# Kernel optimization log

Measured on AMD Instinct MI355X. Metric: run time of the kernel, lower is better.

Reference implementation:

```python
import jax, jax.numpy as jnp
import numpy as np

B = 4096
D1 = 2048   # APPEARANCE_DIM
D2 = 1024   # POSE_DIM
DF = 8192   # FUSED_DIM
LN_EPS = 1e-5
L2_EPS = 1e-12


def setup_inputs() -> dict:
    key = jax.random.key(0)
    ks = jax.random.split(key, 6)
    x = jax.random.normal(ks[0], (B, D1), dtype=jnp.float32)
    y = jax.random.normal(ks[1], (B, D2), dtype=jnp.float32)
    h1 = jax.random.randint(ks[2], (D1,), 0, DF, dtype=jnp.int32)
    h2 = jax.random.randint(ks[3], (D2,), 0, DF, dtype=jnp.int32)
    s1 = (2 * jax.random.randint(ks[4], (D1,), 0, 2) - 1).astype(jnp.float32)
    s2 = (2 * jax.random.randint(ks[5], (D2,), 0, 2) - 1).astype(jnp.float32)
    gamma = jnp.ones((DF,), dtype=jnp.float32)
    beta = jnp.zeros((DF,), dtype=jnp.float32)
    return {"x": x, "y": y, "s1": s1, "s2": s2, "gamma": gamma,
            "beta": beta, "h1": h1, "h2": h2}


def count_sketch(v, h, s, out_dim):
    # v: [B, Din], h: [Din] int indices into out_dim, s: [Din] +-1 signs
    # single vectorized scatter-add along the feature axis
    return jnp.zeros((v.shape[0], out_dim), v.dtype).at[:, h].add(v * s)


def reference(x, y, s1, s2, gamma, beta, h1, h2):
    x_sk = count_sketch(x, h1, s1, DF)          # [B, DF]
    y_sk = count_sketch(y, h2, s2, DF)          # [B, DF]
    # circular convolution via FFT
    fused = jnp.fft.ifft(jnp.fft.fft(x_sk, axis=1) * jnp.fft.fft(y_sk, axis=1),
                         axis=1).real           # [B, DF]
    # LayerNorm over last dim
    mu = jnp.mean(fused, axis=-1, keepdims=True)
    var = jnp.mean(jnp.square(fused - mu), axis=-1, keepdims=True)
    normed = (fused - mu) * jax.lax.rsqrt(var + LN_EPS) * gamma + beta
    # F.normalize(p=2, dim=1)
    nrm = jnp.linalg.norm(normed, axis=1, keepdims=True)
    return normed / jnp.maximum(nrm, L2_EPS)
```

## Files before the change

kernel.cpp:

```cpp
#include <hip/hip_runtime.h>
#include <math.h>

#define BATCH 4096
#define D1 2048
#define D2 1024
#define DF 8192
#define NT 512

#define PADI(i) ((i) + ((i) >> 5))

__device__ __forceinline__ float2 cmul(float2 a, float2 b) {
    return make_float2(a.x * b.x - a.y * b.y, a.x * b.y + a.y * b.x);
}
__device__ __forceinline__ float2 cadd(float2 a, float2 b) { return make_float2(a.x + b.x, a.y + b.y); }
__device__ __forceinline__ float2 csub(float2 a, float2 b) { return make_float2(a.x - b.x, a.y - b.y); }

#define RT_C 0.92387953251128674f
#define RT_S 0.38268343236508977f
#define RT_H 0.70710678118654752f

__device__ __forceinline__ float2 rootF(int j) {
    switch (j & 7) {
        case 0:  return make_float2( 1.f,   0.f  );
        case 1:  return make_float2( RT_C, -RT_S );
        case 2:  return make_float2( RT_H, -RT_H );
        case 3:  return make_float2( RT_S, -RT_C );
        case 4:  return make_float2( 0.f,  -1.f  );
        case 5:  return make_float2(-RT_S, -RT_C );
        case 6:  return make_float2(-RT_H, -RT_H );
        default: return make_float2(-RT_C, -RT_S );
    }
}
__device__ __forceinline__ float2 rootI(int j) {
    float2 r = rootF(j);
    return make_float2(r.x, -r.y);
}

__device__ __forceinline__ int brev4c(int x) {
    return ((x & 1) << 3) | ((x & 2) << 1) | ((x & 4) >> 1) | ((x & 8) >> 3);
}
__device__ __forceinline__ int brev9(int x) {
    return (int)(__brev((unsigned)x) >> 23);
}

__device__ __forceinline__ void fft16_dif(float2 v[16], float2 wb) {
    const float2 wb2 = cmul(wb, wb);
    const float2 wb4 = cmul(wb2, wb2);
    const float2 wb8 = cmul(wb4, wb4);
    #pragma unroll
    for (int m = 0; m < 8; ++m) {
        float2 W = cmul(wb, rootF(m));
        float2 a = v[m], b = v[m + 8];
        v[m] = cadd(a, b);
        v[m + 8] = cmul(csub(a, b), W);
    }
    #pragma unroll
    for (int g = 0; g < 2; ++g)
        #pragma unroll
        for (int m = 0; m < 4; ++m) {
            int i = 8 * g + m;
            float2 W = cmul(wb2, rootF(2 * m));
            float2 a = v[i], b = v[i + 4];
            v[i] = cadd(a, b);
            v[i + 4] = cmul(csub(a, b), W);
        }
    #pragma unroll
    for (int g = 0; g < 4; ++g)
        #pragma unroll
        for (int m = 0; m < 2; ++m) {
            int i = 4 * g + m;
            float2 W = cmul(wb4, rootF(4 * m));
            float2 a = v[i], b = v[i + 2];
            v[i] = cadd(a, b);
            v[i + 2] = cmul(csub(a, b), W);
        }
    #pragma unroll
    for (int g = 0; g < 8; ++g) {
        int i = 2 * g;
        float2 a = v[i], b = v[i + 1];
        v[i] = cadd(a, b);
        v[i + 1] = cmul(csub(a, b), wb8);
    }
}

__device__ __forceinline__ void fft16_dit(float2 v[16], float2 wb) {
    const float2 wb2 = cmul(wb, wb);
    const float2 wb4 = cmul(wb2, wb2);
    const float2 wb8 = cmul(wb4, wb4);
    #pragma unroll
    for (int g = 0; g < 8; ++g) {
        int i = 2 * g;
        float2 a = v[i], b = cmul(v[i + 1], wb8);
        v[i] = cadd(a, b);
        v[i + 1] = csub(a, b);
    }
    #pragma unroll
    for (int g = 0; g < 4; ++g)
        #pragma unroll
        for (int m = 0; m < 2; ++m) {
            int i = 4 * g + m;
            float2 W = cmul(wb4, rootI(4 * m));
            float2 a = v[i], b = cmul(v[i + 2], W);
            v[i] = cadd(a, b);
            v[i + 2] = csub(a, b);
        }
    #pragma unroll
    for (int g = 0; g < 2; ++g)
        #pragma unroll
        for (int m = 0; m < 4; ++m) {
            int i = 8 * g + m;
            float2 W = cmul(wb2, rootI(2 * m));
            float2 a = v[i], b = cmul(v[i + 4], W);
            v[i] = cadd(a, b);
            v[i + 4] = csub(a, b);
        }
    #pragma unroll
    for (int m = 0; m < 8; ++m) {
        float2 W = cmul(wb, rootI(m));
        float2 a = v[m], b = cmul(v[m + 8], W);
        v[m] = cadd(a, b);
        v[m + 8] = csub(a, b);
    }
}

__global__ __launch_bounds__(NT, 4)
void mcb_fused2(const float* __restrict__ x, const float* __restrict__ y,
                const float* __restrict__ s1, const float* __restrict__ s2,
                const float* __restrict__ gamma, const float* __restrict__ beta,
                const int* __restrict__ h1, const int* __restrict__ h2,
                float* __restrict__ out)
{
    __shared__ float re[DF + DF / 32];
    __shared__ float im[DF + DF / 32];
    const int t = threadIdx.x;
    const int row = blockIdx.x;

    #pragma unroll
    for (int m = 0; m < 16; ++m) {
        int p = PADI(t + NT * m);
        re[p] = 0.f; im[p] = 0.f;
    }
    __syncthreads();

    {
        const float* xr = x + (size_t)row * D1;
        #pragma unroll
        for (int c = 0; c < D1 / NT; ++c) {
            int i = t + NT * c;
            atomicAdd(&re[PADI(h1[i])], xr[i] * s1[i]);
        }
        const float* yr = y + (size_t)row * D2;
        #pragma unroll
        for (int c = 0; c < D2 / NT; ++c) {
            int i = t + NT * c;
            atomicAdd(&im[PADI(h2[i])], yr[i] * s2[i]);
        }
    }
    __syncthreads();

    float2 v[16];
    float sn, cs;

    #pragma unroll
    for (int m = 0; m < 16; ++m) {
        int p = PADI(t + 512 * m);
        v[m] = make_float2(re[p], im[p]);
    }
    __sincosf(-(float)M_PI / 4096.f * (float)t, &sn, &cs);
    fft16_dif(v, make_float2(cs, sn));
    #pragma unroll
    for (int m = 0; m < 16; ++m) {
        int p = PADI(t + 512 * m);
        re[p] = v[m].x; im[p] = v[m].y;
    }
    __syncthreads();

    {
        const int lo = t & 31, hi = t >> 5;
        #pragma unroll
        for (int m = 0; m < 16; ++m) {
            int p = PADI(lo + 32 * m + 512 * hi);
            v[m] = make_float2(re[p], im[p]);
        }
        __sincosf(-(float)M_PI / 256.f * (float)lo, &sn, &cs);
        fft16_dif(v, make_float2(cs, sn));
        #pragma unroll
        for (int m = 0; m < 16; ++m) {
            int p = PADI(lo + 32 * m + 512 * hi);
            re[p] = v[m].x; im[p] = v[m].y;
        }
    }
    __syncthreads();

    {
        const int lo = t & 1, hi = t >> 1;
        #pragma unroll
        for (int m = 0; m < 16; ++m) {
            int p = PADI(lo + 2 * m + 32 * hi);
            v[m] = make_float2(re[p], im[p]);
        }
        __sincosf(-(float)M_PI / 16.f * (float)lo, &sn, &cs);
        fft16_dif(v, make_float2(cs, sn));
        #pragma unroll
        for (int m = 0; m < 16; ++m) {
            int p = PADI(lo + 2 * m + 32 * hi);
            re[p] = v[m].x; im[p] = v[m].y;
        }
    }
    __syncthreads();

    #pragma unroll
    for (int m = 0; m < 16; ++m) {
        int p = PADI(16 * t + m);
        v[m] = make_float2(re[p], im[p]);
    }
    #pragma unroll
    for (int g = 0; g < 8; ++g) {
        float2 a = v[2 * g], b = v[2 * g + 1];
        v[2 * g] = cadd(a, b);
        v[2 * g + 1] = csub(a, b);
    }
    #pragma unroll
    for (int m = 0; m < 16; ++m) {
        int p = PADI(16 * t + m);
        re[p] = v[m].x; im[p] = v[m].y;
    }
    __syncthreads();

    {
        const float invN = 1.f / (float)DF;
        const int R = brev9(t);
        const int c2 = (R == 0) ? 0 : brev9(512 - R);
        #pragma unroll
        for (int m = 0; m < 16; ++m) {
            int M = brev4c(m);
            int M2 = (R == 0) ? ((16 - M) & 15) : (15 - M);
            int p2 = PADI(16 * c2 + brev4c(M2));
            float2 a = v[m];
            float2 b = make_float2(re[p2], im[p2]);
            float Xr = 0.5f * (a.x + b.x), Xi = 0.5f * (a.y - b.y);
            float Yr = 0.5f * (a.y + b.y), Yi = 0.5f * (b.x - a.x);
            v[m] = make_float2((Xr * Yr - Xi * Yi) * invN,
                               (Xr * Yi + Xi * Yr) * invN);
        }
        fft16_dit(v, make_float2(1.f, 0.f));
    }
    __syncthreads();
    #pragma unroll
    for (int m = 0; m < 16; ++m) {
        int p = PADI(16 * t + m);
        re[p] = v[m].x; im[p] = v[m].y;
    }
    __syncthreads();

    {
        const int lo = t & 15, hi = t >> 4;
        #pragma unroll
        for (int m = 0; m < 16; ++m) {
            int p = PADI(lo + 16 * m + 256 * hi);
            v[m] = make_float2(re[p], im[p]);
        }
        __sincosf((float)M_PI / 128.f * (float)lo, &sn, &cs);
        fft16_dit(v, make_float2(cs, sn));
        #pragma unroll
        for (int m = 0; m < 16; ++m) {
            int p = PADI(lo + 16 * m + 256 * hi);
            re[p] = v[m].x; im[p] = v[m].y;
        }
    }
    __syncthreads();

    {
        const int lo = t & 255, hi = t >> 8;
        #pragma unroll
        for (int m = 0; m < 16; ++m) {
            int p = PADI(lo + 256 * m + 4096 * hi);
            v[m] = make_float2(re[p], im[p]);
        }
        __sincosf((float)M_PI / 2048.f * (float)lo, &sn, &cs);
        fft16_dit(v, make_float2(cs, sn));
        #pragma unroll
        for (int m = 0; m < 16; ++m) {
            int p = PADI(lo + 256 * m + 4096 * hi);
            re[p] = v[m].x; im[p] = v[m].y;
        }
    }
    __syncthreads();

    #pragma unroll
    for (int m = 0; m < 16; ++m) {
        int p = PADI(t + 512 * m);
        v[m] = make_float2(re[p], im[p]);
    }
    __sincosf((float)M_PI / 4096.f * (float)t, &sn, &cs);
    {
        float2 wb = make_float2(cs, sn);
        #pragma unroll
        for (int m = 0; m < 8; ++m) {
            float2 W = cmul(wb, rootI(m));
            float2 a = v[m], b = cmul(v[m + 8], W);
            v[m] = cadd(a, b);
            v[m + 8] = csub(a, b);
        }
    }

    float lsum = 0.f, lsq = 0.f;
    #pragma unroll
    for (int m = 0; m < 16; ++m) { float f = v[m].x; lsum += f; lsq += f * f; }
    #pragma unroll
    for (int k = 32; k >= 1; k >>= 1) { lsum += __shfl_xor(lsum, k); lsq += __shfl_xor(lsq, k); }
    const int wid = t >> 6, lane = t & 63;
    __syncthreads();
    if (lane == 0) { re[wid] = lsum; re[8 + wid] = lsq; }
    __syncthreads();
    float tsum = 0.f, tsq = 0.f;
    #pragma unroll
    for (int w = 0; w < 8; ++w) { tsum += re[w]; tsq += re[8 + w]; }
    const float mu = tsum * (1.f / (float)DF);
    const float var = tsq * (1.f / (float)DF) - mu * mu;
    const float rstd = rsqrtf(var + 1e-5f);

    float lsq2 = 0.f;
    #pragma unroll
    for (int m = 0; m < 16; ++m) {
        int i = t + 512 * m;
        float nv = (v[m].x - mu) * rstd * gamma[i] + beta[i];
        v[m].x = nv;
        lsq2 += nv * nv;
    }
    #pragma unroll
    for (int k = 32; k >= 1; k >>= 1) lsq2 += __shfl_xor(lsq2, k);
    if (lane == 0) re[16 + wid] = lsq2;
    __syncthreads();
    float t2 = 0.f;
    #pragma unroll
    for (int w = 0; w < 8; ++w) t2 += re[16 + w];
    const float inv = 1.f / fmaxf(sqrtf(t2), 1e-12f);

    float* orow = out + (size_t)row * DF;
    #pragma unroll
    for (int m = 0; m < 16; ++m)
        orow[t + 512 * m] = v[m].x * inv;
}

extern "C" void kernel_launch(void* const* d_in, const int* in_sizes, int n_in,
                              void* d_out, int out_size, void* d_ws, size_t ws_size,
                              hipStream_t stream) {
    const float* x     = (const float*)d_in[0];
    const float* y     = (const float*)d_in[1];
    const float* s1    = (const float*)d_in[2];
    const float* s2    = (const float*)d_in[3];
    const float* gamma = (const float*)d_in[4];
    const float* beta  = (const float*)d_in[5];
    const int*   h1    = (const int*)d_in[6];
    const int*   h2    = (const int*)d_in[7];
    float* out = (float*)d_out;

    hipLaunchKernelGGL(mcb_fused2, dim3(BATCH), dim3(NT), 0, stream,
                       x, y, s1, s2, gamma, beta, h1, h2, out);
}
```

Before: 195.3 us.

## Use half-length real-output inverse FFT and interleaved swizzled shared memory

The inverse transform now exploits the real-valued output. Even and odd samples are packed into a 4096-point complex IFFT, done as radix-8 stages (three plus a spectrum-combine step) instead of the full 8192-point radix-16 inverse. Shared memory moves from padded split re/im arrays to one interleaved float2 array with an XOR swizzle, which allows vectorized float4 and float2 loads. Global loads and stores of inputs, gamma, beta and the output are also widened. The aim is to cut inverse-FFT arithmetic, LDS traffic and barrier stages, at the cost of a more intricate conjugate-pairing step that is sensitive to index mistakes.

Result: faster. 180.3 us (-7.7%).

```diff
diff --git a/kernel.cpp b/kernel.cpp
--- a/kernel.cpp
+++ b/kernel.cpp
@@ -1,19 +1,17 @@
 #include <hip/hip_runtime.h>
 #include <math.h>
 
-#define BATCH 4096
-#define D1 2048
-#define D2 1024
 #define DF 8192
 #define NT 512
 
-#define PADI(i) ((i) + ((i) >> 5))
+#define PH(i) ((i) ^ (((i) >> 5) & 14))
 
 __device__ __forceinline__ float2 cmul(float2 a, float2 b) {
     return make_float2(a.x * b.x - a.y * b.y, a.x * b.y + a.y * b.x);
 }
 __device__ __forceinline__ float2 cadd(float2 a, float2 b) { return make_float2(a.x + b.x, a.y + b.y); }
 __device__ __forceinline__ float2 csub(float2 a, float2 b) { return make_float2(a.x - b.x, a.y - b.y); }
+__device__ __forceinline__ float2 cmuli(float2 a) { return make_float2(-a.y, a.x); }
 
 #define RT_C 0.92387953251128674f
 #define RT_S 0.38268343236508977f
@@ -36,12 +34,7 @@
     return make_float2(r.x, -r.y);
 }
 
-__device__ __forceinline__ int brev4c(int x) {
-    return ((x & 1) << 3) | ((x & 2) << 1) | ((x & 4) >> 1) | ((x & 8) >> 3);
-}
-__device__ __forceinline__ int brev9(int x) {
-    return (int)(__brev((unsigned)x) >> 23);
-}
+__device__ __forceinline__ int brev9(int x) { return (int)(__brev((unsigned)x) >> 23); }
 
 __device__ __forceinline__ void fft16_dif(float2 v[16], float2 wb) {
     const float2 wb2 = cmul(wb, wb);
@@ -83,264 +76,258 @@
     }
 }
 
-__device__ __forceinline__ void fft16_dit(float2 v[16], float2 wb) {
-    const float2 wb2 = cmul(wb, wb);
-    const float2 wb4 = cmul(wb2, wb2);
-    const float2 wb8 = cmul(wb4, wb4);
-    #pragma unroll
-    for (int g = 0; g < 8; ++g) {
-        int i = 2 * g;
-        float2 a = v[i], b = cmul(v[i + 1], wb8);
-        v[i] = cadd(a, b);
-        v[i + 1] = csub(a, b);
-    }
-    #pragma unroll
-    for (int g = 0; g < 4; ++g)
-        #pragma unroll
-        for (int m = 0; m < 2; ++m) {
-            int i = 4 * g + m;
-            float2 W = cmul(wb4, rootI(4 * m));
-            float2 a = v[i], b = cmul(v[i + 2], W);
-            v[i] = cadd(a, b);
-            v[i + 2] = csub(a, b);
-        }
-    #pragma unroll
-    for (int g = 0; g < 2; ++g)
-        #pragma unroll
-        for (int m = 0; m < 4; ++m) {
-            int i = 8 * g + m;
-            float2 W = cmul(wb2, rootI(2 * m));
-            float2 a = v[i], b = cmul(v[i + 4], W);
-            v[i] = cadd(a, b);
-            v[i + 4] = csub(a, b);
-        }
-    #pragma unroll
-    for (int m = 0; m < 8; ++m) {
-        float2 W = cmul(wb, rootI(m));
-        float2 a = v[m], b = cmul(v[m + 8], W);
-        v[m] = cadd(a, b);
-        v[m + 8] = csub(a, b);
-    }
+__device__ __forceinline__ void bf_dit(float2& a, float2& b, float2 W) {
+    float2 bw = cmul(b, W);
+    float2 ta = a;
+    a = cadd(ta, bw);
+    b = csub(ta, bw);
+}
+__device__ __forceinline__ void bf_dit1(float2& a, float2& b) {
+    float2 tb = b, ta = a;
+    a = cadd(ta, tb);
+    b = csub(ta, tb);
+}
+__device__ __forceinline__ void bf_diti(float2& a, float2& b) {
+    float2 bw = cmuli(b);
+    float2 ta = a;
+    a = cadd(ta, bw);
+    b = csub(ta, bw);
+}
+
+__device__ __forceinline__ void fft8_dit(float2 v[8], float2 wq) {
+    const float2 wq2 = cmul(wq, wq);
+    const float2 wq4 = cmul(wq2, wq2);
+    #pragma unroll
+    for (int g = 0; g < 4; ++g) bf_dit(v[2 * g], v[2 * g + 1], wq4);
+    #pragma unroll
+    for (int g = 0; g < 2; ++g) {
+        bf_dit(v[4 * g],     v[4 * g + 2], wq2);
+        bf_dit(v[4 * g + 1], v[4 * g + 3], cmuli(wq2));
+    }
+    bf_dit(v[0], v[4], wq);
+    bf_dit(v[1], v[5], cmul(wq, make_float2(RT_H, RT_H)));
+    bf_dit(v[2], v[6], cmuli(wq));
+    bf_dit(v[3], v[7], cmul(wq, make_float2(-RT_H, RT_H)));
+}
+
+__device__ __forceinline__ void fft8_dit1(float2 v[8]) {
+    #pragma unroll
+    for (int g = 0; g < 4; ++g) bf_dit1(v[2 * g], v[2 * g + 1]);
+    #pragma unroll
+    for (int g = 0; g < 2; ++g) {
+        bf_dit1(v[4 * g],     v[4 * g + 2]);
+        bf_diti(v[4 * g + 1], v[4 * g + 3]);
+    }
+    bf_dit1(v[0], v[4]);
+    bf_dit (v[1], v[5], make_float2(RT_H, RT_H));
+    bf_diti(v[2], v[6]);
+    bf_dit (v[3], v[7], make_float2(-RT_H, RT_H));
 }
 
 __global__ __launch_bounds__(NT, 4)
-void mcb_fused2(const float* __restrict__ x, const float* __restrict__ y,
-                const float* __restrict__ s1, const float* __restrict__ s2,
-                const float* __restrict__ gamma, const float* __restrict__ beta,
-                const int* __restrict__ h1, const int* __restrict__ h2,
-                float* __restrict__ out)
+void mcb3(const float* __restrict__ x, const float* __restrict__ y,
+          const float* __restrict__ s1, const float* __restrict__ s2,
+          const float* __restrict__ gamma, const float* __restrict__ beta,
+          const int* __restrict__ h1, const int* __restrict__ h2,
+          float* __restrict__ out)
 {
-    __shared__ float re[DF + DF / 32];
-    __shared__ float im[DF + DF / 32];
+    __shared__ float2 z[DF];
     const int t = threadIdx.x;
     const int row = blockIdx.x;
 
     #pragma unroll
-    for (int m = 0; m < 16; ++m) {
-        int p = PADI(t + NT * m);
-        re[p] = 0.f; im[p] = 0.f;
-    }
-    __syncthreads();
-
-    {
-        const float* xr = x + (size_t)row * D1;
-        #pragma unroll
-        for (int c = 0; c < D1 / NT; ++c) {
-            int i = t + NT * c;
-            atomicAdd(&re[PADI(h1[i])], xr[i] * s1[i]);
-        }
-        const float* yr = y + (size_t)row * D2;
-        #pragma unroll
-        for (int c = 0; c < D2 / NT; ++c) {
-            int i = t + NT * c;
-            atomicAdd(&im[PADI(h2[i])], yr[i] * s2[i]);
-        }
-    }
-    __syncthreads();
-
-    float2 v[16];
+    for (int m = 0; m < 16; ++m) z[t + NT * m] = make_float2(0.f, 0.f);
+    __syncthreads();
+
+    {
+        const float4* x4  = (const float4*)(x + (size_t)row * 2048);
+        const float4* s14 = (const float4*)s1;
+        const int4*   h14 = (const int4*)h1;
+        float4 xv = x4[t], sv = s14[t];
+        int4 hv = h14[t];
+        atomicAdd(&z[PH(hv.x)].x, xv.x * sv.x);
+        atomicAdd(&z[PH(hv.y)].x, xv.y * sv.y);
+        atomicAdd(&z[PH(hv.z)].x, xv.z * sv.z);
+        atomicAdd(&z[PH(hv.w)].x, xv.w * sv.w);
+        const float2* y2  = (const float2*)(y + (size_t)row * 1024);
+        const float2* s22 = (const float2*)s2;
+        const int2*   h22 = (const int2*)h2;
+        float2 yv = y2[t], tv = s22[t];
+        int2 hw = h22[t];
+        atomicAdd(&z[PH(hw.x)].y, yv.x * tv.x);
+        atomicAdd(&z[PH(hw.y)].y, yv.y * tv.y);
+    }
+    __syncthreads();
+
     float sn, cs;
 
-    #pragma unroll
-    for (int m = 0; m < 16; ++m) {
-        int p = PADI(t + 512 * m);
-        v[m] = make_float2(re[p], im[p]);
-    }
-    __sincosf(-(float)M_PI / 4096.f * (float)t, &sn, &cs);
-    fft16_dif(v, make_float2(cs, sn));
-    #pragma unroll
-    for (int m = 0; m < 16; ++m) {
-        int p = PADI(t + 512 * m);
-        re[p] = v[m].x; im[p] = v[m].y;
+    {
+        float2 v[16];
+        #pragma unroll
+        for (int m = 0; m < 16; ++m) v[m] = z[PH(t + 512 * m)];
+        __sincosf(-(float)M_PI / 4096.f * (float)t, &sn, &cs);
+        fft16_dif(v, make_float2(cs, sn));
+        #pragma unroll
+        for (int m = 0; m < 16; ++m) z[PH(t + 512 * m)] = v[m];
     }
     __syncthreads();
 
     {
         const int lo = t & 31, hi = t >> 5;
-        #pragma unroll
-        for (int m = 0; m < 16; ++m) {
-            int p = PADI(lo + 32 * m + 512 * hi);
-            v[m] = make_float2(re[p], im[p]);
-        }
+        float2 v[16];
+        #pragma unroll
+        for (int m = 0; m < 16; ++m) v[m] = z[PH(lo + 32 * m + 512 * hi)];
         __sincosf(-(float)M_PI / 256.f * (float)lo, &sn, &cs);
         fft16_dif(v, make_float2(cs, sn));
         #pragma unroll
-        for (int m = 0; m < 16; ++m) {
-            int p = PADI(lo + 32 * m + 512 * hi);
-            re[p] = v[m].x; im[p] = v[m].y;
-        }
+        for (int m = 0; m < 16; ++m) z[PH(lo + 32 * m + 512 * hi)] = v[m];
     }
     __syncthreads();
 
     {
         const int lo = t & 1, hi = t >> 1;
-        #pragma unroll
-        for (int m = 0; m < 16; ++m) {
-            int p = PADI(lo + 2 * m + 32 * hi);
-            v[m] = make_float2(re[p], im[p]);
-        }
+        float2 v[16];
+        #pragma unroll
+        for (int m = 0; m < 16; ++m) v[m] = z[PH(lo + 2 * m + 32 * hi)];
         __sincosf(-(float)M_PI / 16.f * (float)lo, &sn, &cs);
         fft16_dif(v, make_float2(cs, sn));
         #pragma unroll
-        for (int m = 0; m < 16; ++m) {
-            int p = PADI(lo + 2 * m + 32 * hi);
-            re[p] = v[m].x; im[p] = v[m].y;
-        }
-    }
-    __syncthreads();
-
-    #pragma unroll
-    for (int m = 0; m < 16; ++m) {
-        int p = PADI(16 * t + m);
-        v[m] = make_float2(re[p], im[p]);
-    }
-    #pragma unroll
-    for (int g = 0; g < 8; ++g) {
-        float2 a = v[2 * g], b = v[2 * g + 1];
-        v[2 * g] = cadd(a, b);
-        v[2 * g + 1] = csub(a, b);
-    }
-    #pragma unroll
-    for (int m = 0; m < 16; ++m) {
-        int p = PADI(16 * t + m);
-        re[p] = v[m].x; im[p] = v[m].y;
-    }
-    __syncthreads();
-
-    {
-        const float invN = 1.f / (float)DF;
-        const int R = brev9(t);
-        const int c2 = (R == 0) ? 0 : brev9(512 - R);
-        #pragma unroll
-        for (int m = 0; m < 16; ++m) {
-            int M = brev4c(m);
-            int M2 = (R == 0) ? ((16 - M) & 15) : (15 - M);
-            int p2 = PADI(16 * c2 + brev4c(M2));
-            float2 a = v[m];
-            float2 b = make_float2(re[p2], im[p2]);
-            float Xr = 0.5f * (a.x + b.x), Xi = 0.5f * (a.y - b.y);
-            float Yr = 0.5f * (a.y + b.y), Yi = 0.5f * (b.x - a.x);
-            v[m] = make_float2((Xr * Yr - Xi * Yi) * invN,
-                               (Xr * Yi + Xi * Yr) * invN);
-        }
-        fft16_dit(v, make_float2(1.f, 0.f));
-    }
-    __syncthreads();
-    #pragma unroll
-    for (int m = 0; m < 16; ++m) {
-        int p = PADI(16 * t + m);
-        re[p] = v[m].x; im[p] = v[m].y;
-    }
-    __syncthreads();
-
-    {
-        const int lo = t & 15, hi = t >> 4;
-        #pragma unroll
-        for (int m = 0; m < 16; ++m) {
-            int p = PADI(lo + 16 * m + 256 * hi);
-            v[m] = make_float2(re[p], im[p]);
-        }
-        __sincosf((float)M_PI / 128.f * (float)lo, &sn, &cs);
-        fft16_dit(v, make_float2(cs, sn));
-        #pragma unroll
-        for (int m = 0; m < 16; ++m) {
-            int p = PADI(lo + 16 * m + 256 * hi);
-            re[p] = v[m].x; im[p] = v[m].y;
-        }
-    }
-    __syncthreads();
-
-    {
-        const int lo = t & 255, hi = t >> 8;
-        #pragma unroll
-        for (int m = 0; m < 16; ++m) {
-            int p = PADI(lo + 256 * m + 4096 * hi);
-            v[m] = make_float2(re[p], im[p]);
-        }
-        __sincosf((float)M_PI / 2048.f * (float)lo, &sn, &cs);
-        fft16_dit(v, make_float2(cs, sn));
-        #pragma unroll
-        for (int m = 0; m < 16; ++m) {
-            int p = PADI(lo + 256 * m + 4096 * hi);
-            re[p] = v[m].x; im[p] = v[m].y;
-        }
-    }
-    __syncthreads();
-
-    #pragma unroll
-    for (int m = 0; m < 16; ++m) {
-        int p = PADI(t + 512 * m);
-        v[m] = make_float2(re[p], im[p]);
-    }
-    __sincosf((float)M_PI / 4096.f * (float)t, &sn, &cs);
-    {
-        float2 wb = make_float2(cs, sn);
+        for (int m = 0; m < 16; ++m) z[PH(lo + 2 * m + 32 * hi)] = v[m];
+    }
+    __syncthreads();
+
+    float2 u8[8];
+    {
+        const int R  = brev9(t);
+        const int tp = brev9((512 - R) & 511);
+        float2 a[8], b[8], pa[8], pb[8];
         #pragma unroll
         for (int m = 0; m < 8; ++m) {
-            float2 W = cmul(wb, rootI(m));
-            float2 a = v[m], b = cmul(v[m + 8], W);
-            v[m] = cadd(a, b);
-            v[m + 8] = csub(a, b);
-        }
-    }
+            float4 q = *(const float4*)&z[PH(16 * t + 2 * m)];
+            a[m] = make_float2(q.x, q.y);  b[m] = make_float2(q.z, q.w);
+            float4 qp = *(const float4*)&z[PH(16 * tp + 2 * (7 - m))];
+            pa[m] = make_float2(qp.x, qp.y); pb[m] = make_float2(qp.z, qp.w);
+        }
+        #pragma unroll
+        for (int m = 0; m < 8; ++m) {
+            float2 ta = a[m],  tb = b[m];
+            a[m] = cadd(ta, tb);  b[m] = csub(ta, tb);
+            ta = pa[m]; tb = pb[m];
+            pa[m] = cadd(ta, tb); pb[m] = csub(ta, tb);
+        }
+        if (t == 0) {
+            float2 ca[8], cb[8];
+            #pragma unroll
+            for (int m = 0; m < 8; ++m) { ca[m] = a[m]; cb[m] = b[m]; }
+            const int tbl[8] = {0, 1, 3, 2, 7, 6, 5, 4};
+            #pragma unroll
+            for (int m = 0; m < 8; ++m) {
+                if (m == 0) { pa[0] = cb[0]; pb[0] = ca[0]; }
+                else        { pa[m] = ca[tbl[m]]; pb[m] = cb[tbl[m]]; }
+            }
+        }
+        __sincosf((float)M_PI / 4096.f * (float)R, &sn, &cs);
+        const float2 wR = make_float2(cs, sn);
+        const float invN = 1.f / 8192.f;
+        const int MB[8] = {0, 4, 2, 6, 1, 5, 3, 7};
+        #pragma unroll
+        for (int m = 0; m < 8; ++m) {
+            float2 A = a[m], B = b[m], A2 = pa[m], B2 = pb[m];
+            float X1r = 0.5f * (A.x + B2.x), X1i = 0.5f * (A.y - B2.y);
+            float Y1r = 0.5f * (A.y + B2.y), Y1i = 0.5f * (B2.x - A.x);
+            float2 P1 = make_float2((X1r * Y1r - X1i * Y1i) * invN,
+                                    (X1r * Y1i + X1i * Y1r) * invN);
+            float X2r = 0.5f * (B.x + A2.x), X2i = 0.5f * (B.y - A2.y);
+            float Y2r = 0.5f * (B.y + A2.y), Y2i = 0.5f * (A2.x - B.x);
+            float2 P2 = make_float2((X2r * Y2r - X2i * Y2i) * invN,
+                                    (X2r * Y2i + X2i * Y2r) * invN);
+            float2 S = cadd(P1, P2);
+            float2 D = csub(P1, P2);
+            float2 Dw = cmul(D, cmul(wR, rootI(MB[m])));
+            u8[m] = make_float2(S.x - Dw.y, S.y + Dw.x);
+        }
+        fft8_dit1(u8);
+        __syncthreads();
+        #pragma unroll
+        for (int g = 0; g < 4; ++g) {
+            *(float4*)&z[PH(8 * t + 2 * g)] =
+                make_float4(u8[2 * g].x, u8[2 * g].y, u8[2 * g + 1].x, u8[2 * g + 1].y);
+        }
+    }
+    __syncthreads();
+
+    {
+        const int lo = t & 7, hi = t >> 3;
+        #pragma unroll
+        for (int m = 0; m < 8; ++m) u8[m] = z[PH(lo + 8 * m + 64 * hi)];
+        __sincosf((float)M_PI / 32.f * (float)lo, &sn, &cs);
+        fft8_dit(u8, make_float2(cs, sn));
+        #pragma unroll
+        for (int m = 0; m < 8; ++m) z[PH(lo + 8 * m + 64 * hi)] = u8[m];
+    }
+    __syncthreads();
+
+    {
+        const int lo = t & 63, hi = t >> 6;
+        #pragma unroll
+        for (int m = 0; m < 8; ++m) u8[m] = z[PH(lo + 64 * m + 512 * hi)];
+        __sincosf((float)M_PI / 256.f * (float)lo, &sn, &cs);
+        fft8_dit(u8, make_float2(cs, sn));
+        #pragma unroll
+        for (int m = 0; m < 8; ++m) z[PH(lo + 64 * m + 512 * hi)] = u8[m];
+    }
+    __syncthreads();
+
+    #pragma unroll
+    for (int m = 0; m < 8; ++m) u8[m] = z[PH(t + 512 * m)];
+    __sincosf((float)M_PI / 2048.f * (float)t, &sn, &cs);
+    fft8_dit(u8, make_float2(cs, sn));
 
     float lsum = 0.f, lsq = 0.f;
     #pragma unroll
-    for (int m = 0; m < 16; ++m) { float f = v[m].x; lsum += f; lsq += f * f; }
+    for (int m = 0; m < 8; ++m) {
+        lsum += u8[m].x + u8[m].y;
+        lsq  += u8[m].x * u8[m].x + u8[m].y * u8[m].y;
+    }
     #pragma unroll
     for (int k = 32; k >= 1; k >>= 1) { lsum += __shfl_xor(lsum, k); lsq += __shfl_xor(lsq, k); }
     const int wid = t >> 6, lane = t & 63;
     __syncthreads();
-    if (lane == 0) { re[wid] = lsum; re[8 + wid] = lsq; }
+    if (lane == 0) z[wid] = make_float2(lsum, lsq);
     __syncthreads();
     float tsum = 0.f, tsq = 0.f;
     #pragma unroll
-    for (int w = 0; w < 8; ++w) { tsum += re[w]; tsq += re[8 + w]; }
-    const float mu = tsum * (1.f / (float)DF);
-    const float var = tsq * (1.f / (float)DF) - mu * mu;
+    for (int w = 0; w < 8; ++w) { tsum += z[w].x; tsq += z[w].y; }
+    const float mu   = tsum * (1.f / (float)DF);
+    const float var  = tsq * (1.f / (float)DF) - mu * mu;
     const float rstd = rsqrtf(var + 1e-5f);
 
+    const float2* g2  = (const float2*)gamma;
+    const float2* bt2 = (const float2*)beta;
+    float2 nv[8];
     float lsq2 = 0.f;
     #pragma unroll
-    for (int m = 0; m < 16; ++m) {
+    for (int m = 0; m < 8; ++m) {
         int i = t + 512 * m;
-        float nv = (v[m].x - mu) * rstd * gamma[i] + beta[i];
-        v[m].x = nv;
-        lsq2 += nv * nv;
+        float2 g = g2[i], bb = bt2[i];
+        float ne = (u8[m].x - mu) * rstd * g.x + bb.x;
+        float no = (u8[m].y - mu) * rstd * g.y + bb.y;
+        nv[m] = make_float2(ne, no);
+        lsq2 += ne * ne + no * no;
     }
     #pragma unroll
     for (int k = 32; k >= 1; k >>= 1) lsq2 += __shfl_xor(lsq2, k);
-    if (lane == 0) re[16 + wid] = lsq2;
+    if (lane == 0) z[8 + wid].x = lsq2;
     __syncthreads();
     float t2 = 0.f;
     #pragma unroll
-    for (int w = 0; w < 8; ++w) t2 += re[16 + w];
+    for (int w = 0; w < 8; ++w) t2 += z[8 + w].x;
     const float inv = 1.f / fmaxf(sqrtf(t2), 1e-12f);
 
-    float* orow = out + (size_t)row * DF;
-    #pragma unroll
-    for (int m = 0; m < 16; ++m)
-        orow[t + 512 * m] = v[m].x * inv;
+    float2* o2 = (float2*)(out + (size_t)row * DF);
+    #pragma unroll
+    for (int m = 0; m < 8; ++m)
+        o2[t + 512 * m] = make_float2(nv[m].x * inv, nv[m].y * inv);
 }
 
 extern "C" void kernel_launch(void* const* d_in, const int* in_sizes, int n_in,
@@ -356,6 +343,6 @@
     const int*   h2    = (const int*)d_in[7];
     float* out = (float*)d_out;
 
-    hipLaunchKernelGGL(mcb_fused2, dim3(BATCH), dim3(NT), 0, stream,
+    hipLaunchKernelGGL(mcb3, dim3(4096), dim3(NT), 0, stream,
                        x, y, s1, s2, gamma, beta, h1, h2, out);
 }
```
